# Optimization experiments

Hardware: AMD Instinct MI355X
Metric: run time of the kernel (lower is better)

## Reference

```python
import jax, jax.numpy as jnp
import numpy as np

OUT, IN = 4096, 4096
NNZ = 838860  # 0.05 * OUT * IN
ALPHA = 1.0   # set_privacy(True)


def setup_inputs() -> dict:
    key = jax.random.key(0)
    k1, k2, k3, k4, k5, k6 = jax.random.split(key, 6)
    x = jax.random.normal(k1, (2, 2048, IN), dtype=jnp.float32)
    # packed uint4 pairs stored as bytes (kept in int32 per spec; values in [0,256))
    base_packed = jax.random.randint(k2, (OUT, IN // 2), 0, 256, dtype=jnp.int32)
    # per-row dequant scales (positive, small, like ceiling/7)
    scales = jax.random.uniform(k3, (OUT, 1), dtype=jnp.float32, minval=1e-3, maxval=5e-2)
    ortho_vals = jax.random.normal(k4, (NNZ,), dtype=jnp.float32) * 0.02
    ortho_rows = jax.random.randint(k5, (NNZ,), 0, OUT, dtype=jnp.int32)
    ortho_cols = jax.random.randint(k6, (NNZ,), 0, IN, dtype=jnp.int32)
    return {"x": x, "base_packed": base_packed, "scales": scales,
            "ortho_vals": ortho_vals, "ortho_rows": ortho_rows, "ortho_cols": ortho_cols}


def _dequant(base_packed, scales):
    # unpack two int4 values per byte: col 2k <- low nibble, col 2k+1 <- high nibble
    p = base_packed.astype(jnp.int32)
    low = p & 0xF
    high = (p >> 4) & 0xF
    O, K = p.shape
    w_int4 = jnp.stack([low, high], axis=-1).reshape(O, 2 * K) - 8  # offset-binary -> [-8, 7]
    return w_int4.astype(jnp.float32) * scales  # [O, I]


def reference(x, base_packed, scales, ortho_vals, ortho_rows, ortho_cols):
    O = base_packed.shape[0]
    I = 2 * base_packed.shape[1]
    w_base = _dequant(base_packed, scales)  # [O, I] fp32
    # sparse outlier residual scattered into dense weight (CSR spmm equivalent)
    w_corr = jnp.zeros((O, I), jnp.float32).at[ortho_rows, ortho_cols].add(ortho_vals)
    w = w_base + ALPHA * w_corr
    x_flat = x.reshape(-1, I).astype(jnp.float32)
    out = x_flat @ w.T  # [N, O]
    return out.reshape(x.shape[:-1] + (O,)).astype(x.dtype)
```

## Files before the change

### kernel.cpp

```cpp
#include <hip/hip_runtime.h>
#include <cstdint>
#include <cstddef>

typedef __bf16 bf16x8 __attribute__((ext_vector_type(8)));
typedef float f32x4 __attribute__((ext_vector_type(4)));
typedef unsigned short ushort8 __attribute__((ext_vector_type(8)));

#define OUT_DIM 4096
#define IN_DIM 4096
#define NT 64


__device__ __forceinline__ unsigned short f2bf(float f) {
  unsigned u = __float_as_uint(f);
  return (unsigned short)((u + 0x7FFFu + ((u >> 16) & 1u)) >> 16);
}

__device__ __forceinline__ void async_copy16(const void* g, void* l) {
  __builtin_amdgcn_global_load_lds(
      (const __attribute__((address_space(1))) unsigned int*)g,
      (__attribute__((address_space(3))) unsigned int*)l, 16, 0, 0);
}


__global__ __launch_bounds__(256) void dequant_kernel(
    const int* __restrict__ packed, const float* __restrict__ scales,
    unsigned short* __restrict__ wb) {
  int idx = blockIdx.x * 256 + threadIdx.x;
  int4 p = reinterpret_cast<const int4*>(packed)[idx];
  float s = scales[idx >> 9];
  ushort8 o;
  o[0] = f2bf((float)((p.x & 15) - 8) * s);
  o[1] = f2bf((float)(((p.x >> 4) & 15) - 8) * s);
  o[2] = f2bf((float)((p.y & 15) - 8) * s);
  o[3] = f2bf((float)(((p.y >> 4) & 15) - 8) * s);
  o[4] = f2bf((float)((p.z & 15) - 8) * s);
  o[5] = f2bf((float)(((p.z >> 4) & 15) - 8) * s);
  o[6] = f2bf((float)((p.w & 15) - 8) * s);
  o[7] = f2bf((float)(((p.w >> 4) & 15) - 8) * s);
  *reinterpret_cast<ushort8*>(&wb[(size_t)idx * 8]) = o;
}

__global__ __launch_bounds__(256) void scatter_bf16_kernel(
    const float* __restrict__ vals, const int* __restrict__ rows,
    const int* __restrict__ cols, unsigned short* __restrict__ wb, int nnz) {
  int i = blockIdx.x * 256 + threadIdx.x;
  if (i >= nnz) return;
  size_t idx = (size_t)rows[i] * IN_DIM + cols[i];
  unsigned int* word = (unsigned int*)(wb + (idx & ~(size_t)1));
  const bool hi = (idx & 1) != 0;
  const float v = vals[i];
  unsigned int old = *word, assumed;
  do {
    assumed = old;
    unsigned short h = hi ? (unsigned short)(assumed >> 16)
                          : (unsigned short)(assumed & 0xFFFFu);
    float f = __uint_as_float((unsigned)h << 16);
    unsigned short nh = f2bf(f + v);
    unsigned int nw = hi ? ((assumed & 0x0000FFFFu) | ((unsigned)nh << 16))
                         : ((assumed & 0xFFFF0000u) | (unsigned)nh);
    old = atomicCAS(word, assumed, nw);
  } while (old != assumed);
}

__global__ __launch_bounds__(256) void cvt_kernel(
    const float* __restrict__ in, unsigned short* __restrict__ out) {
  int i = blockIdx.x * 256 + threadIdx.x;
  float4 a = reinterpret_cast<const float4*>(in)[2 * i];
  float4 b = reinterpret_cast<const float4*>(in)[2 * i + 1];
  ushort8 o;
  o[0] = f2bf(a.x); o[1] = f2bf(a.y); o[2] = f2bf(a.z); o[3] = f2bf(a.w);
  o[4] = f2bf(b.x); o[5] = f2bf(b.y); o[6] = f2bf(b.z); o[7] = f2bf(b.w);
  *reinterpret_cast<ushort8*>(&out[(size_t)i * 8]) = o;
}


#define SLABOFF(buf, op, kh) ((((buf) * 4) + ((op) * 2) + (kh)) * 8192)

#define STAGE(buf, op, kh, kt)                                              \
  do {                                                                      \
    const unsigned short* g_ = ((op) ? gB : gA) + (kt) * 64 + (kh) * 32;    \
    unsigned short* l_ = (unsigned short*)lds + SLABOFF(buf, op, kh) + wave * 512; \
    async_copy16(g_, l_);                                                   \
    async_copy16(g_ + 128 * IN_DIM, l_ + 4096);                             \
  } while (0)

#define MFMA_ __builtin_amdgcn_mfma_f32_16x16x32_bf16

#define PHASE(BUF, KS, MH, READB, STAGEST, DOWAIT)                          \
  do {                                                                      \
    const unsigned short* as_ = (const unsigned short*)lds + SLABOFF(BUF, 0, KS); \
    bf16x8 a0_ = *(const bf16x8*)(as_ + offA[(MH) * 4 + 0]);                \
    bf16x8 a1_ = *(const bf16x8*)(as_ + offA[(MH) * 4 + 1]);                \
    bf16x8 a2_ = *(const bf16x8*)(as_ + offA[(MH) * 4 + 2]);                \
    bf16x8 a3_ = *(const bf16x8*)(as_ + offA[(MH) * 4 + 3]);                \
    if (READB) {                                                            \
      const unsigned short* bs_ = (const unsigned short*)lds + SLABOFF(BUF, 1, KS); \
      bB0 = *(const bf16x8*)(bs_ + offB[0]);                                \
      bB1 = *(const bf16x8*)(bs_ + offB[1]);                                \
      bB2 = *(const bf16x8*)(bs_ + offB[2]);                                \
      bB3 = *(const bf16x8*)(bs_ + offB[3]);                                \
    }                                                                       \
    STAGEST;                                                                \
    if (DOWAIT) asm volatile("s_waitcnt vmcnt(8)" ::: "memory");            \
    __builtin_amdgcn_s_barrier();                                           \
    asm volatile("s_waitcnt lgkmcnt(0)" ::: "memory");                      \
    __builtin_amdgcn_sched_barrier(0);                                      \
    __builtin_amdgcn_s_setprio(1);                                          \
    acc[(MH) * 4 + 0][0] = MFMA_(a0_, bB0, acc[(MH) * 4 + 0][0], 0, 0, 0);  \
    acc[(MH) * 4 + 0][1] = MFMA_(a0_, bB1, acc[(MH) * 4 + 0][1], 0, 0, 0);  \
    acc[(MH) * 4 + 0][2] = MFMA_(a0_, bB2, acc[(MH) * 4 + 0][2], 0, 0, 0);  \
    acc[(MH) * 4 + 0][3] = MFMA_(a0_, bB3, acc[(MH) * 4 + 0][3], 0, 0, 0);  \
    acc[(MH) * 4 + 1][0] = MFMA_(a1_, bB0, acc[(MH) * 4 + 1][0], 0, 0, 0);  \
    acc[(MH) * 4 + 1][1] = MFMA_(a1_, bB1, acc[(MH) * 4 + 1][1], 0, 0, 0);  \
    acc[(MH) * 4 + 1][2] = MFMA_(a1_, bB2, acc[(MH) * 4 + 1][2], 0, 0, 0);  \
    acc[(MH) * 4 + 1][3] = MFMA_(a1_, bB3, acc[(MH) * 4 + 1][3], 0, 0, 0);  \
    acc[(MH) * 4 + 2][0] = MFMA_(a2_, bB0, acc[(MH) * 4 + 2][0], 0, 0, 0);  \
    acc[(MH) * 4 + 2][1] = MFMA_(a2_, bB1, acc[(MH) * 4 + 2][1], 0, 0, 0);  \
    acc[(MH) * 4 + 2][2] = MFMA_(a2_, bB2, acc[(MH) * 4 + 2][2], 0, 0, 0);  \
    acc[(MH) * 4 + 2][3] = MFMA_(a2_, bB3, acc[(MH) * 4 + 2][3], 0, 0, 0);  \
    acc[(MH) * 4 + 3][0] = MFMA_(a3_, bB0, acc[(MH) * 4 + 3][0], 0, 0, 0);  \
    acc[(MH) * 4 + 3][1] = MFMA_(a3_, bB1, acc[(MH) * 4 + 3][1], 0, 0, 0);  \
    acc[(MH) * 4 + 3][2] = MFMA_(a3_, bB2, acc[(MH) * 4 + 3][2], 0, 0, 0);  \
    acc[(MH) * 4 + 3][3] = MFMA_(a3_, bB3, acc[(MH) * 4 + 3][3], 0, 0, 0);  \
    __builtin_amdgcn_s_setprio(0);                                          \
    __builtin_amdgcn_s_barrier();                                           \
  } while (0)

#define MINC(x) ((x) < NT ? (x) : (NT - 1))

#define TILE(BUF, t)                                                        \
  do {                                                                      \
    PHASE(BUF, 0, 0, true, STAGE(1 - (BUF), 0, 1, MINC((t) + 1)), false);   \
    PHASE(BUF, 0, 1, false, STAGE(1 - (BUF), 1, 1, MINC((t) + 1)), true);   \
    PHASE(BUF, 1, 0, true, STAGE(BUF, 0, 0, MINC((t) + 2)), false);         \
    PHASE(BUF, 1, 1, false, STAGE(BUF, 1, 0, MINC((t) + 2)), true);         \
  } while (0)

__global__ __launch_bounds__(512, 2) void gemm_kernel(
    const unsigned short* __restrict__ A,
    const unsigned short* __restrict__ B,
    float* __restrict__ C) {
  __shared__ __align__(16) unsigned short lds[65536];

  const int bid = blockIdx.x;
  const int xcd = bid & 7, i_ = bid >> 3;
  const int bm = (xcd >> 1) * 4 + (i_ >> 3);
  const int bn = (xcd & 1) * 8 + (i_ & 7);
  const int m0 = bm * 256, n0 = bn * 256;

  const int tid = threadIdx.x;
  const int wave = tid >> 6, lane = tid & 63;
  const int wm = wave >> 2, wn = wave & 3;
  const int lrow = lane & 15, lk = lane >> 4;

  const int r0 = tid >> 2, s0 = tid & 3;
  const int s0s = s0 ^ ((r0 >> 1) & 3);
  const unsigned short* gA = A + (size_t)(m0 + r0) * IN_DIM + s0s * 8;
  const unsigned short* gB = B + (size_t)(n0 + r0) * IN_DIM + s0s * 8;

  const int lks = lk ^ ((lrow >> 1) & 3);
  int offA[8], offB[4];
#pragma unroll
  for (int i = 0; i < 8; ++i) offA[i] = (wm * 128 + i * 16 + lrow) * 32 + lks * 8;
#pragma unroll
  for (int i = 0; i < 4; ++i) offB[i] = (wn * 64 + i * 16 + lrow) * 32 + lks * 8;

  f32x4 acc[8][4];
#pragma unroll
  for (int mi = 0; mi < 8; ++mi)
#pragma unroll
    for (int ni = 0; ni < 4; ++ni) acc[mi][ni] = (f32x4){0.f, 0.f, 0.f, 0.f};

  STAGE(0, 0, 0, 0); STAGE(0, 1, 0, 0);
  asm volatile("" ::: "memory");
  STAGE(0, 0, 1, 0); STAGE(0, 1, 1, 0);
  asm volatile("" ::: "memory");
  STAGE(1, 0, 0, 1); STAGE(1, 1, 0, 1);
  asm volatile("s_waitcnt vmcnt(8)" ::: "memory");
  __builtin_amdgcn_s_barrier();

  bf16x8 bB0, bB1, bB2, bB3;
#pragma unroll 1
  for (int p = 0; p < NT / 2; ++p) {
    const int te = 2 * p;
    TILE(0, te);
    TILE(1, te + 1);
  }
  asm volatile("s_waitcnt vmcnt(0)" ::: "memory");

#pragma unroll
  for (int mi = 0; mi < 8; ++mi)
#pragma unroll
    for (int ni = 0; ni < 4; ++ni) {
      int m = m0 + wm * 128 + mi * 16 + lk * 4;
      int n = n0 + wn * 64 + ni * 16 + lrow;
      float* cp = &C[(size_t)m * OUT_DIM + n];
#pragma unroll
      for (int r = 0; r < 4; ++r) cp[(size_t)r * OUT_DIM] = acc[mi][ni][r];
    }
}


extern "C" void kernel_launch(void* const* d_in, const int* in_sizes, int n_in,
                              void* d_out, int out_size, void* d_ws, size_t ws_size,
                              hipStream_t stream) {
  const float* x      = (const float*)d_in[0];
  const int*   packed = (const int*)d_in[1];
  const float* scales = (const float*)d_in[2];
  const float* vals   = (const float*)d_in[3];
  const int*   rows   = (const int*)d_in[4];
  const int*   cols   = (const int*)d_in[5];
  float* out = (float*)d_out;

  const int nnz = in_sizes[3];

  char* ws = (char*)d_ws;
  const size_t MB = 1024 * 1024;
  unsigned short* Wb = (unsigned short*)ws;
  unsigned short* Xb = (unsigned short*)(ws + 32 * MB);

  dequant_kernel<<<8192, 256, 0, stream>>>(packed, scales, Wb);
  scatter_bf16_kernel<<<(nnz + 255) / 256, 256, 0, stream>>>(vals, rows, cols, Wb, nnz);
  cvt_kernel<<<8192, 256, 0, stream>>>(x, Xb);
  gemm_kernel<<<256, 512, 0, stream>>>(Xb, Wb, out);
}
```

Baseline: 187.8 us.

## Prefetch next phase's LDS fragments into registers during MFMA blocks

The GEMM main loop now keeps two register sets of A/B fragments (even and odd). Each phase issues the LDS reads for the following phase just before its 16 MFMAs, so LDS latency overlaps the matrix math instead of sitting in front of it. Addressing is also simplified: byte offsets from one lane base, and B's global pointer is derived from A plus a single byte delta. This roughly doubles the live fragment registers, which adds VGPR pressure on top of the 128-register accumulator at 512 threads with two blocks per CU.

```diff
diff --git a/kernel.cpp b/kernel.cpp
--- a/kernel.cpp
+++ b/kernel.cpp
@@ -75,54 +75,62 @@
 }
 
 
-#define SLABOFF(buf, op, kh) ((((buf) * 4) + ((op) * 2) + (kh)) * 8192)
+#define SB(buf, op, kh) ((((buf) * 4) + ((op) * 2) + (kh)) * 16384)
 
 #define STAGE(buf, op, kh, kt)                                              \
   do {                                                                      \
-    const unsigned short* g_ = ((op) ? gB : gA) + (kt) * 64 + (kh) * 32;    \
-    unsigned short* l_ = (unsigned short*)lds + SLABOFF(buf, op, kh) + wave * 512; \
+    const unsigned short* gsrc_ =                                           \
+        (op) ? (const unsigned short*)((const char*)gA + dBA) : gA;         \
+    const unsigned short* g_ = gsrc_ + (kt) * 64 + (kh) * 32;               \
+    unsigned short* l_ =                                                    \
+        (unsigned short*)((char*)lds + SB(buf, op, kh)) + wave * 512;       \
     async_copy16(g_, l_);                                                   \
     async_copy16(g_ + 128 * IN_DIM, l_ + 4096);                             \
   } while (0)
 
 #define MFMA_ __builtin_amdgcn_mfma_f32_16x16x32_bf16
 
-#define PHASE(BUF, KS, MH, READB, STAGEST, DOWAIT)                          \
+#define LDA4(d0, d1, d2, d3, BUF, KS, MH)                                   \
+  d0 = *(const bf16x8*)(ldsc + (laneA + SB(BUF, 0, KS) + (MH) * 4096 + 0)); \
+  d1 = *(const bf16x8*)(ldsc + (laneA + SB(BUF, 0, KS) + (MH) * 4096 + 1024)); \
+  d2 = *(const bf16x8*)(ldsc + (laneA + SB(BUF, 0, KS) + (MH) * 4096 + 2048)); \
+  d3 = *(const bf16x8*)(ldsc + (laneA + SB(BUF, 0, KS) + (MH) * 4096 + 3072))
+
+#define LDB4(d0, d1, d2, d3, BUF, KS)                                       \
+  d0 = *(const bf16x8*)(ldsc + (laneB + SB(BUF, 1, KS) + 0));               \
+  d1 = *(const bf16x8*)(ldsc + (laneB + SB(BUF, 1, KS) + 1024));            \
+  d2 = *(const bf16x8*)(ldsc + (laneB + SB(BUF, 1, KS) + 2048));            \
+  d3 = *(const bf16x8*)(ldsc + (laneB + SB(BUF, 1, KS) + 3072))
+
+#define MM16(MH, A0, A1, A2, A3, B0, B1, B2, B3)                            \
+  acc[(MH) * 4 + 0][0] = MFMA_(A0, B0, acc[(MH) * 4 + 0][0], 0, 0, 0);      \
+  acc[(MH) * 4 + 0][1] = MFMA_(A0, B1, acc[(MH) * 4 + 0][1], 0, 0, 0);      \
+  acc[(MH) * 4 + 0][2] = MFMA_(A0, B2, acc[(MH) * 4 + 0][2], 0, 0, 0);      \
+  acc[(MH) * 4 + 0][3] = MFMA_(A0, B3, acc[(MH) * 4 + 0][3], 0, 0, 0);      \
+  acc[(MH) * 4 + 1][0] = MFMA_(A1, B0, acc[(MH) * 4 + 1][0], 0, 0, 0);      \
+  acc[(MH) * 4 + 1][1] = MFMA_(A1, B1, acc[(MH) * 4 + 1][1], 0, 0, 0);      \
+  acc[(MH) * 4 + 1][2] = MFMA_(A1, B2, acc[(MH) * 4 + 1][2], 0, 0, 0);      \
+  acc[(MH) * 4 + 1][3] = MFMA_(A1, B3, acc[(MH) * 4 + 1][3], 0, 0, 0);      \
+  acc[(MH) * 4 + 2][0] = MFMA_(A2, B0, acc[(MH) * 4 + 2][0], 0, 0, 0);      \
+  acc[(MH) * 4 + 2][1] = MFMA_(A2, B1, acc[(MH) * 4 + 2][1], 0, 0, 0);      \
+  acc[(MH) * 4 + 2][2] = MFMA_(A2, B2, acc[(MH) * 4 + 2][2], 0, 0, 0);      \
+  acc[(MH) * 4 + 2][3] = MFMA_(A2, B3, acc[(MH) * 4 + 2][3], 0, 0, 0);      \
+  acc[(MH) * 4 + 3][0] = MFMA_(A3, B0, acc[(MH) * 4 + 3][0], 0, 0, 0);      \
+  acc[(MH) * 4 + 3][1] = MFMA_(A3, B1, acc[(MH) * 4 + 3][1], 0, 0, 0);      \
+  acc[(MH) * 4 + 3][2] = MFMA_(A3, B2, acc[(MH) * 4 + 3][2], 0, 0, 0);      \
+  acc[(MH) * 4 + 3][3] = MFMA_(A3, B3, acc[(MH) * 4 + 3][3], 0, 0, 0)
+
+#define PHASEX(STAGEST, DOWAIT, MH, A0, A1, A2, A3, B0, B1, B2, B3, ...)    \
   do {                                                                      \
-    const unsigned short* as_ = (const unsigned short*)lds + SLABOFF(BUF, 0, KS); \
-    bf16x8 a0_ = *(const bf16x8*)(as_ + offA[(MH) * 4 + 0]);                \
-    bf16x8 a1_ = *(const bf16x8*)(as_ + offA[(MH) * 4 + 1]);                \
-    bf16x8 a2_ = *(const bf16x8*)(as_ + offA[(MH) * 4 + 2]);                \
-    bf16x8 a3_ = *(const bf16x8*)(as_ + offA[(MH) * 4 + 3]);                \
-    if (READB) {                                                            \
-      const unsigned short* bs_ = (const unsigned short*)lds + SLABOFF(BUF, 1, KS); \
-      bB0 = *(const bf16x8*)(bs_ + offB[0]);                                \
-      bB1 = *(const bf16x8*)(bs_ + offB[1]);                                \
-      bB2 = *(const bf16x8*)(bs_ + offB[2]);                                \
-      bB3 = *(const bf16x8*)(bs_ + offB[3]);                                \
-    }                                                                       \
     STAGEST;                                                                \
     if (DOWAIT) asm volatile("s_waitcnt vmcnt(8)" ::: "memory");            \
     __builtin_amdgcn_s_barrier();                                           \
     asm volatile("s_waitcnt lgkmcnt(0)" ::: "memory");                      \
     __builtin_amdgcn_sched_barrier(0);                                      \
+    __VA_ARGS__;                                                            \
+    __builtin_amdgcn_sched_barrier(0);                                      \
     __builtin_amdgcn_s_setprio(1);                                          \
-    acc[(MH) * 4 + 0][0] = MFMA_(a0_, bB0, acc[(MH) * 4 + 0][0], 0, 0, 0);  \
-    acc[(MH) * 4 + 0][1] = MFMA_(a0_, bB1, acc[(MH) * 4 + 0][1], 0, 0, 0);  \
-    acc[(MH) * 4 + 0][2] = MFMA_(a0_, bB2, acc[(MH) * 4 + 0][2], 0, 0, 0);  \
-    acc[(MH) * 4 + 0][3] = MFMA_(a0_, bB3, acc[(MH) * 4 + 0][3], 0, 0, 0);  \
-    acc[(MH) * 4 + 1][0] = MFMA_(a1_, bB0, acc[(MH) * 4 + 1][0], 0, 0, 0);  \
-    acc[(MH) * 4 + 1][1] = MFMA_(a1_, bB1, acc[(MH) * 4 + 1][1], 0, 0, 0);  \
-    acc[(MH) * 4 + 1][2] = MFMA_(a1_, bB2, acc[(MH) * 4 + 1][2], 0, 0, 0);  \
-    acc[(MH) * 4 + 1][3] = MFMA_(a1_, bB3, acc[(MH) * 4 + 1][3], 0, 0, 0);  \
-    acc[(MH) * 4 + 2][0] = MFMA_(a2_, bB0, acc[(MH) * 4 + 2][0], 0, 0, 0);  \
-    acc[(MH) * 4 + 2][1] = MFMA_(a2_, bB1, acc[(MH) * 4 + 2][1], 0, 0, 0);  \
-    acc[(MH) * 4 + 2][2] = MFMA_(a2_, bB2, acc[(MH) * 4 + 2][2], 0, 0, 0);  \
-    acc[(MH) * 4 + 2][3] = MFMA_(a2_, bB3, acc[(MH) * 4 + 2][3], 0, 0, 0);  \
-    acc[(MH) * 4 + 3][0] = MFMA_(a3_, bB0, acc[(MH) * 4 + 3][0], 0, 0, 0);  \
-    acc[(MH) * 4 + 3][1] = MFMA_(a3_, bB1, acc[(MH) * 4 + 3][1], 0, 0, 0);  \
-    acc[(MH) * 4 + 3][2] = MFMA_(a3_, bB2, acc[(MH) * 4 + 3][2], 0, 0, 0);  \
-    acc[(MH) * 4 + 3][3] = MFMA_(a3_, bB3, acc[(MH) * 4 + 3][3], 0, 0, 0);  \
+    MM16(MH, A0, A1, A2, A3, B0, B1, B2, B3);                               \
     __builtin_amdgcn_s_setprio(0);                                          \
     __builtin_amdgcn_s_barrier();                                           \
   } while (0)
@@ -131,10 +139,20 @@
 
 #define TILE(BUF, t)                                                        \
   do {                                                                      \
-    PHASE(BUF, 0, 0, true, STAGE(1 - (BUF), 0, 1, MINC((t) + 1)), false);   \
-    PHASE(BUF, 0, 1, false, STAGE(1 - (BUF), 1, 1, MINC((t) + 1)), true);   \
-    PHASE(BUF, 1, 0, true, STAGE(BUF, 0, 0, MINC((t) + 2)), false);         \
-    PHASE(BUF, 1, 1, false, STAGE(BUF, 1, 0, MINC((t) + 2)), true);         \
+    PHASEX(STAGE(1 - (BUF), 0, 1, MINC((t) + 1)), 0, 0,                     \
+           aE0, aE1, aE2, aE3, bE0, bE1, bE2, bE3,                          \
+           LDA4(aO0, aO1, aO2, aO3, BUF, 0, 1));                            \
+    PHASEX(STAGE(1 - (BUF), 1, 1, MINC((t) + 1)), 1, 1,                     \
+           aO0, aO1, aO2, aO3, bE0, bE1, bE2, bE3,                          \
+           LDA4(aE0, aE1, aE2, aE3, BUF, 1, 0);                             \
+           LDB4(bO0, bO1, bO2, bO3, BUF, 1));                               \
+    PHASEX(STAGE(BUF, 0, 0, MINC((t) + 2)), 0, 0,                           \
+           aE0, aE1, aE2, aE3, bO0, bO1, bO2, bO3,                          \
+           LDA4(aO0, aO1, aO2, aO3, BUF, 1, 1));                            \
+    PHASEX(STAGE(BUF, 1, 0, MINC((t) + 2)), 1, 1,                           \
+           aO0, aO1, aO2, aO3, bO0, bO1, bO2, bO3,                          \
+           LDA4(aE0, aE1, aE2, aE3, 1 - (BUF), 0, 0);                       \
+           LDB4(bE0, bE1, bE2, bE3, 1 - (BUF), 0));                         \
   } while (0)
 
 __global__ __launch_bounds__(512, 2) void gemm_kernel(
@@ -142,6 +160,7 @@
     const unsigned short* __restrict__ B,
     float* __restrict__ C) {
   __shared__ __align__(16) unsigned short lds[65536];
+  const char* ldsc = (const char*)lds;
 
   const int bid = blockIdx.x;
   const int xcd = bid & 7, i_ = bid >> 3;
@@ -157,20 +176,21 @@
   const int r0 = tid >> 2, s0 = tid & 3;
   const int s0s = s0 ^ ((r0 >> 1) & 3);
   const unsigned short* gA = A + (size_t)(m0 + r0) * IN_DIM + s0s * 8;
-  const unsigned short* gB = B + (size_t)(n0 + r0) * IN_DIM + s0s * 8;
+  const ptrdiff_t dBA = ((const char*)B - (const char*)A) +
+                        (ptrdiff_t)(n0 - m0) * IN_DIM * 2;
 
   const int lks = lk ^ ((lrow >> 1) & 3);
-  int offA[8], offB[4];
-#pragma unroll
-  for (int i = 0; i < 8; ++i) offA[i] = (wm * 128 + i * 16 + lrow) * 32 + lks * 8;
-#pragma unroll
-  for (int i = 0; i < 4; ++i) offB[i] = (wn * 64 + i * 16 + lrow) * 32 + lks * 8;
+  const int laneA = (wm * 128 + lrow) * 64 + lks * 16;
+  const int laneB = (wn * 64 + lrow) * 64 + lks * 16;
 
   f32x4 acc[8][4];
 #pragma unroll
   for (int mi = 0; mi < 8; ++mi)
 #pragma unroll
     for (int ni = 0; ni < 4; ++ni) acc[mi][ni] = (f32x4){0.f, 0.f, 0.f, 0.f};
+
+  bf16x8 aE0, aE1, aE2, aE3, aO0, aO1, aO2, aO3;
+  bf16x8 bE0, bE1, bE2, bE3, bO0, bO1, bO2, bO3;
 
   STAGE(0, 0, 0, 0); STAGE(0, 1, 0, 0);
   asm volatile("" ::: "memory");
@@ -180,7 +200,9 @@
   asm volatile("s_waitcnt vmcnt(8)" ::: "memory");
   __builtin_amdgcn_s_barrier();
 
-  bf16x8 bB0, bB1, bB2, bB3;
+  LDA4(aE0, aE1, aE2, aE3, 0, 0, 0);
+  LDB4(bE0, bE1, bE2, bE3, 0, 0);
+
 #pragma unroll 1
   for (int p = 0; p < NT / 2; ++p) {
     const int te = 2 * p;
```

New measurement: 188.4 us. Within noise of the previous version (+0.3%).
